# Optimization experiments

Hardware: AMD Instinct MI355X
Metric: run time of the kernel (lower is better)

Reference implementation:

```python
import jax, jax.numpy as jnp
import numpy as np
import math

B, L = 16, 100
NC = 80
STRIDES = (8.0, 16.0, 32.0)
ANCHORS = np.array([[10., 13.], [16., 30.], [33., 23.], [30., 61.], [62., 45.],
                    [59., 119.], [116., 90.], [156., 198.], [373., 326.]], np.float32)
ANCH_MASKS = ((0, 1, 2), (3, 4, 5), (6, 7, 8))
THRESH = 4.0          # gt_match_max_ratio
CIOU_RATIO = 1.0
W_BOX, W_OBJ, W_CLS = 0.05, 1.0, 0.58
OV = 0.5              # overlap in assign_targets_to_proposals


def _bce(x, z):
    # binary_cross_entropy_with_logits, elementwise
    return -(z * jax.nn.log_sigmoid(x) + (1.0 - z) * jax.nn.log_sigmoid(-x))


def _ciou_xywh(b1, b2, eps=1e-9):
    # b1, b2: [M,4] center-x, center-y, w, h  (matches _bbox_iou with x1y1x2y2=False, CIoU=True)
    b1x1, b1x2 = b1[:, 0] - b1[:, 2] / 2, b1[:, 0] + b1[:, 2] / 2
    b1y1, b1y2 = b1[:, 1] - b1[:, 3] / 2, b1[:, 1] + b1[:, 3] / 2
    b2x1, b2x2 = b2[:, 0] - b2[:, 2] / 2, b2[:, 0] + b2[:, 2] / 2
    b2y1, b2y2 = b2[:, 1] - b2[:, 3] / 2, b2[:, 1] + b2[:, 3] / 2
    inter = jnp.clip(jnp.minimum(b1x2, b2x2) - jnp.maximum(b1x1, b2x1), 0) * \
            jnp.clip(jnp.minimum(b1y2, b2y2) - jnp.maximum(b1y1, b2y1), 0)
    w1, h1 = b1x2 - b1x1, b1y2 - b1y1 + eps
    w2, h2 = b2x2 - b2x1, b2y2 - b2y1 + eps
    union = w1 * h1 + w2 * h2 - inter + eps
    iou = inter / union
    cw = jnp.maximum(b1x2, b2x2) - jnp.minimum(b1x1, b2x1)
    ch = jnp.maximum(b1y2, b2y2) - jnp.minimum(b1y1, b2y1)
    c2 = cw ** 2 + ch ** 2 + eps
    rho2 = ((b2x1 + b2x2 - b1x1 - b1x2) ** 2 + (b2y1 + b2y2 - b1y1 - b1y2) ** 2) / 4
    v = (4.0 / math.pi ** 2) * (jnp.arctan(w2 / h2) - jnp.arctan(w1 / h1)) ** 2
    alpha = jax.lax.stop_gradient(v / (1.0 + eps - iou + v))  # torch.no_grad()
    return iou - (rho2 / c2 + v * alpha)


def _yolo_loss(y_pred0, y_pred1, y_pred2, y_true):
    # valid GT rows: nlabel counts rows with positive sum; valid rows assumed contiguous at front
    nlabel = (y_true.sum(-1) > 0).sum(-1)                                # [B]
    valid = (jnp.arange(L)[None, :] < nlabel[:, None]).reshape(-1)       # [N]
    batch_ids = jnp.repeat(jnp.arange(B), L)                             # [N]
    flat = y_true.reshape(-1, 5)
    gt_labels = flat[:, 4].astype(jnp.int32)
    # convert x1,y1,w,h -> cx,cy,w,h
    gt_boxes = jnp.concatenate([flat[:, :2] + flat[:, 2:4] / 2, flat[:, 2:4]], axis=1)
    N = B * L
    offsets = jnp.array([[0, 0], [-OV, 0], [0, -OV], [OV, 0], [0, OV]], jnp.float32)
    loss_box = jnp.float32(0.0)
    loss_obj = jnp.float32(0.0)
    loss_cls = jnp.float32(0.0)
    for li, out in enumerate((y_pred0, y_pred1, y_pred2)):
        s = STRIDES[li]
        anch = jnp.asarray(ANCHORS[list(ANCH_MASKS[li])] / s)            # [3,2] grid units
        H, Wd = out.shape[2], out.shape[3]
        nch = 5 + NC
        p = out.reshape(B, -1, nch, H, Wd).transpose(0, 1, 3, 4, 2)      # [B,3,H,W,nch]
        sgb = gt_boxes / s                                               # [N,4]
        # size_matched_idx
        r = sgb[:, None, 2:4] / anch[None]                               # [N,3,2]
        maxr = jnp.maximum(r, 1.0 / r).max(-1)                           # [N,3]
        match = (maxr < THRESH) & valid[:, None]                         # [N,3]
        # assign_targets_to_proposals: 5 offset candidates per (gt, anchor)
        x, y = sgb[:, 0], sgb[:, 1]
        fx, fy = jnp.mod(x, 1.0), jnp.mod(y, 1.0)
        cond = jnp.stack([
            jnp.ones_like(x, bool),
            (x > 1) & (fx < OV),
            (y > 1) & (fy < OV),
            (x < Wd - 1) & (fx > 1 - OV),
            (y < H - 1) & (fy > 1 - OV),
        ], axis=1)                                                       # [N,5]
        coords = (sgb[:, None, :2] + offsets[None]).astype(jnp.int32)    # [N,5,2] (trunc like .long())
        cmask = (match[:, :, None] & cond[:, None, :]).reshape(-1)       # [N*3*5]
        bf = jnp.broadcast_to(batch_ids[:, None, None], (N, 3, 5)).reshape(-1)
        af = jnp.broadcast_to(jnp.arange(3)[None, :, None], (N, 3, 5)).reshape(-1)
        gf = jnp.broadcast_to(jnp.arange(N)[:, None, None], (N, 3, 5)).reshape(-1)
        gxy = jnp.broadcast_to(coords[:, None, :, :], (N, 3, 5, 2)).reshape(-1, 2)
        gx, gy = gxy[:, 0], gxy[:, 1]
        pred = p[bf, af, gy, gx]                                         # [M,nch] (OOB gathers clamped; masked out)
        pxy = jax.nn.sigmoid(pred[:, :2]) + gxy.astype(pred.dtype)
        pwh = jnp.exp(pred[:, 2:4]) * anch[af]
        pbox = jnp.concatenate([pxy, pwh], axis=1)
        ci = _ciou_xywh(pbox, sgb[gf])                                   # [M]
        cm = cmask.astype(pred.dtype)
        nval = cm.sum()
        denom = jnp.maximum(nval, 1.0)
        loss_box = loss_box + jnp.where(nval > 0, ((1.0 - ci) * cm).sum() / denom, 0.0)
        # objectness target scatter (invalid candidates dropped via OOB batch index)
        obj_val = CIOU_RATIO * jnp.clip(ci, 0) + (1.0 - CIOU_RATIO)
        bs = jnp.where(cmask, bf, B)
        gt_obj = jnp.zeros((B, 3, H, Wd), pred.dtype).at[bs, af, gy, gx].set(obj_val, mode='drop')
        if NC > 1:
            zhot = jax.nn.one_hot(gt_labels[gf], NC, dtype=pred.dtype)
            bce_c = _bce(pred[:, 5:], zhot)
            loss_cls = loss_cls + jnp.where(nval > 0, (bce_c * cm[:, None]).sum() / (denom * NC), 0.0)
        loss_obj = loss_obj + _bce(p[..., 4], gt_obj).mean()
    lb, lo, lc = W_BOX * loss_box, W_OBJ * loss_obj, W_CLS * loss_cls
    return lb + lo + lc, lb, lo, lc


def setup_inputs():
    rng = np.random.default_rng(0)
    k0, k1, k2 = jax.random.split(jax.random.key(0), 3)
    y_pred0 = jax.random.normal(k0, (B, 3 * (5 + NC), 80, 80), jnp.float32)
    y_pred1 = jax.random.normal(k1, (B, 3 * (5 + NC), 40, 40), jnp.float32)
    y_pred2 = jax.random.normal(k2, (B, 3 * (5 + NC), 20, 20), jnp.float32)
    yt = np.zeros((B, L, 5), np.float32)
    n_valid = 70  # valid labels contiguous at the front, rest zero-padded
    yt[:, :n_valid, 0] = rng.uniform(1.0, 560.0, (B, n_valid))
    yt[:, :n_valid, 1] = rng.uniform(1.0, 560.0, (B, n_valid))
    yt[:, :n_valid, 2] = rng.uniform(8.0, 80.0, (B, n_valid))
    yt[:, :n_valid, 3] = rng.uniform(8.0, 80.0, (B, n_valid))
    yt[:, :n_valid, 4] = rng.integers(0, NC, (B, n_valid)).astype(np.float32)
    return {"y_pred0": y_pred0, "y_pred1": y_pred1, "y_pred2": y_pred2, "y_true": jnp.asarray(yt)}


def reference(y_pred0, y_pred1, y_pred2, y_true):
    return _yolo_loss(y_pred0, y_pred1, y_pred2, y_true)
```

## Files before the change

kernel.cpp:

```cpp
#include <hip/hip_runtime.h>
#include <math.h>

#define BB 16
#define LL 100
#define NCLS 80
#define CPB 282
#define CAP 288
#define PREPB 256
#define GATB 4608
#define OBJB 99
#define NTHR 1024

__device__ __constant__ int   d_W[3]     = {80, 40, 20};
__device__ __constant__ int   d_HW[3]    = {6400, 1600, 400};
__device__ __constant__ float d_stride[3]= {8.f, 16.f, 32.f};
__device__ __constant__ int   d_gtoff[3] = {0, 307200, 384000};
__device__ __constant__ float d_anch[3][3][2] = {
  {{10.f,13.f},{16.f,30.f},{33.f,23.f}},
  {{30.f,61.f},{62.f,45.f},{59.f,119.f}},
  {{116.f,90.f},{156.f,198.f},{373.f,326.f}}};

#define ACC_OFF   0
#define CNT_OFF   16
#define CANDG_OFF 272

__device__ __forceinline__ float softplusf(float t) {
  return fmaxf(t, 0.f) + log1pf(expf(-fabsf(t)));
}
__device__ __forceinline__ float sigmoidf_(float x) {
  return 1.f / (1.f + expf(-x));
}

__device__ __forceinline__ float ciou_(float px, float py, float pw, float ph,
                                       float gx, float gy, float gw, float gh) {
  const float eps = 1e-9f;
  float b1x1 = px - pw*0.5f, b1x2 = px + pw*0.5f;
  float b1y1 = py - ph*0.5f, b1y2 = py + ph*0.5f;
  float b2x1 = gx - gw*0.5f, b2x2 = gx + gw*0.5f;
  float b2y1 = gy - gh*0.5f, b2y2 = gy + gh*0.5f;
  float iw = fmaxf(fminf(b1x2,b2x2) - fmaxf(b1x1,b2x1), 0.f);
  float ih = fmaxf(fminf(b1y2,b2y2) - fmaxf(b1y1,b2y1), 0.f);
  float inter = iw*ih;
  float w1 = b1x2-b1x1, h1 = b1y2-b1y1 + eps;
  float w2 = b2x2-b2x1, h2 = b2y2-b2y1 + eps;
  float uni = w1*h1 + w2*h2 - inter + eps;
  float iou = inter/uni;
  float cw = fmaxf(b1x2,b2x2) - fminf(b1x1,b2x1);
  float ch = fmaxf(b1y2,b2y2) - fminf(b1y1,b2y1);
  float c2 = cw*cw + ch*ch + eps;
  float dx = b2x1+b2x2-b1x1-b1x2;
  float dy = b2y1+b2y2-b1y1-b1y2;
  float rho2 = (dx*dx + dy*dy)*0.25f;
  float at = atanf(w2/h2) - atanf(w1/h1);
  float v = (float)(4.0/(M_PI*M_PI)) * at*at;
  float alpha = v / (1.0f + eps - iou + v);
  return iou - (rho2/c2 + v*alpha);
}

__global__ __launch_bounds__(512)
void k_prep(const float* __restrict__ yt, float* __restrict__ acc,
            unsigned int* __restrict__ cntg, unsigned int* __restrict__ candg)
{
  __shared__ int s_nl[2];
  __shared__ int s_cnt;
  const int blk = blockIdx.x, tid = threadIdx.x;

  if (blk == 0 && tid >= 32 && tid < 48) acc[tid-32] = 0.f;

  if (tid < 2)  s_nl[tid] = 0;
  if (tid == 2) s_cnt = 0;

  const int t0 = blk*CPB;
  const int b_lo = t0/4500;
  int b_hi = (t0 + CPB - 1)/4500; if (b_hi > BB-1) b_hi = BB-1;
  __syncthreads();

  if (tid < LL) {
    const float* row = yt + (size_t)(b_lo*LL + tid)*5;
    if (row[0]+row[1]+row[2]+row[3]+row[4] > 0.f) atomicAdd(&s_nl[0], 1);
  } else if (tid >= 128 && tid < 128+LL && b_hi != b_lo) {
    const float* row = yt + (size_t)(b_hi*LL + (tid-128))*5;
    if (row[0]+row[1]+row[2]+row[3]+row[4] > 0.f) atomicAdd(&s_nl[1], 1);
  }
  __syncthreads();

  if (tid < CPB) {
    int t = t0 + tid;
    if (t < BB*LL*45) {
      int b = t/4500; int rem = t - b*4500;
      int g_loc = rem/45; int rem2 = rem - g_loc*45;
      int lvl = rem2/15, ao = rem2 - lvl*15, a = ao/5, o = ao - a*5;
      const float* row = yt + (size_t)(b*LL + g_loc)*5;
      float s = d_stride[lvl];
      int W = d_W[lvl];
      float cx = (row[0] + row[2]*0.5f)/s;
      float cy = (row[1] + row[3]*0.5f)/s;
      float w = row[2]/s, h = row[3]/s;
      float aw = d_anch[lvl][a][0]/s, ah = d_anch[lvl][a][1]/s;
      float rw = w/aw, rh = h/ah;
      float maxr = fmaxf(fmaxf(rw,1.f/rw), fmaxf(rh,1.f/rh));
      int nl = (b == b_lo) ? s_nl[0] : s_nl[1];
      bool m = (g_loc < nl) && (maxr < 4.0f);
      float fx = cx - floorf(cx), fy = cy - floorf(cy);
      bool c;
      switch (o) {
        case 0: c = true; break;
        case 1: c = (cx > 1.f) && (fx < 0.5f); break;
        case 2: c = (cy > 1.f) && (fy < 0.5f); break;
        case 3: c = (cx < (float)(W-1)) && (fx > 0.5f); break;
        default:c = (cy < (float)(W-1)) && (fy > 0.5f); break;
      }
      if (m && c) {
        const float offx[5] = {0.f,-0.5f,0.f,0.5f,0.f};
        const float offy[5] = {0.f,0.f,-0.5f,0.f,0.5f};
        int gx = (int)(cx + offx[o]);
        int gy = (int)(cy + offy[o]);
        int g = b*LL + g_loc;
        unsigned pk = ((unsigned)lvl<<27) | ((unsigned)a<<25) | ((unsigned)g<<14)
                    | ((unsigned)gy<<7) | (unsigned)gx;
        int idx = atomicAdd(&s_cnt, 1);
        candg[blk*CAP + idx] = pk;
      }
    }
  }
  __syncthreads();
  if (tid == 0) cntg[blk] = (unsigned)s_cnt;
}

__global__ __launch_bounds__(NTHR)
void k_gather(const float* __restrict__ p0, const float* __restrict__ p1,
              const float* __restrict__ p2, const float* __restrict__ yt,
              const unsigned int* __restrict__ cntg,
              const unsigned int* __restrict__ candg,
              float* __restrict__ acc)
{
  __shared__ float s_acc[15];
  const int blk = blockIdx.x, tid = threadIdx.x;
  if (tid < 15) s_acc[tid] = 0.f;
  __syncthreads();

  if (blk < GATB) {
    int wg = blk*16 + (tid >> 6);
    int lane = tid & 63;
    int p = wg / CAP;
    int sIdx = wg - p*CAP;
    if (sIdx < (int)cntg[p]) {
      unsigned pk = candg[p*CAP + sIdx];
      int gx  = pk & 127;
      int gy  = (pk>>7) & 127;
      int g   = (pk>>14) & 2047;
      int a   = (pk>>25) & 3;
      int lvl = (pk>>27) & 3;
      int b = g / LL;
      float s = d_stride[lvl];
      int W = d_W[lvl], HW = d_HW[lvl];
      const float* pr = (lvl==0) ? p0 : (lvl==1) ? p1 : p2;
      const float* row = yt + (size_t)g*5;
      float cx = (row[0] + row[2]*0.5f)/s;
      float cy = (row[1] + row[3]*0.5f)/s;
      float w  = row[2]/s, h = row[3]/s;
      int label = (int)row[4];
      float aw = d_anch[lvl][a][0]/s, ah = d_anch[lvl][a][1]/s;

      const float* base = pr + (size_t)((b*255 + a*85)*HW + gy*W + gx);
      float xA = base[(size_t)lane*HW];
      float xB = (lane < 21) ? base[(size_t)(64+lane)*HW] : 0.f;
      float x0 = __shfl(xA,0), x1 = __shfl(xA,1), x2 = __shfl(xA,2), x3 = __shfl(xA,3);
      float xobj = __shfl(xA,4);

      float pxc = sigmoidf_(x0) + (float)gx;
      float pyc = sigmoidf_(x1) + (float)gy;
      float pw = expf(x2)*aw, ph = expf(x3)*ah;
      float ci = ciou_(pxc,pyc,pw,ph, cx,cy,w,h);

      float cls = 0.f;
      if (lane >= 5) { int cc = lane-5;  cls += (cc==label) ? softplusf(-xA) : softplusf(xA); }
      if (lane < 21) { int cc = 59+lane; cls += (cc==label) ? softplusf(-xB) : softplusf(xB); }
      for (int off = 1; off < 64; off <<= 1) cls += __shfl_xor(cls, off);

      if (lane == 0) {
        float bx = 1.f - ci;
        float zx = fmaxf(ci, 0.f) * xobj;
        atomicAdd(&s_acc[lvl],     bx);
        atomicAdd(&s_acc[3+lvl],  cls);
        atomicAdd(&s_acc[6+lvl],  1.f);
        atomicAdd(&s_acc[12+lvl], zx);
      }
    }
  } else {
    int gt = (blk - GATB)*NTHR + tid;
    if (gt < 100800) {
      int e0 = gt*4;
      int lvl = (e0 < 307200) ? 0 : (e0 < 384000 ? 1 : 2);
      int HW = d_HW[lvl];
      int idx = e0 - d_gtoff[lvl];
      int b = idx/(3*HW); int r2 = idx - b*3*HW; int a = r2/HW; int pos = r2 - a*HW;
      const float* pr = (lvl==0) ? p0 : (lvl==1) ? p1 : p2;
      const float4 x4 = *(const float4*)(pr + (size_t)((b*255 + a*85 + 4)*HW + pos));
      float sp = softplusf(x4.x) + softplusf(x4.y) + softplusf(x4.z) + softplusf(x4.w);
      atomicAdd(&s_acc[9+(e0 < 307200 ? 0 : (e0 < 384000 ? 1 : 2))], sp);
    }
  }
  __syncthreads();
  if (tid < 15 && s_acc[tid] != 0.f) atomicAdd(&acc[tid], s_acc[tid]);
}

__global__ __launch_bounds__(64)
void k_fin(const float* __restrict__ acc, float* __restrict__ out) {
  if (threadIdx.x != 0) return;
  const float cells[3] = {307200.f, 76800.f, 19200.f};
  float lb = 0.f, lc = 0.f, lo = 0.f;
  for (int l = 0; l < 3; ++l) {
    float nval  = acc[6+l];
    float denom = fmaxf(nval, 1.f);
    if (nval > 0.f) {
      lb += acc[l] / denom;
      lc += acc[3+l] / (denom * (float)NCLS);
    }
    lo += (acc[9+l] - acc[12+l]) / cells[l];
  }
  lb *= 0.05f;
  lc *= 0.58f;
  out[0] = lb + lo + lc;
  out[1] = lb;
  out[2] = lo;
  out[3] = lc;
}

extern "C" void kernel_launch(void* const* d_in, const int* in_sizes, int n_in,
                              void* d_out, int out_size, void* d_ws, size_t ws_size,
                              hipStream_t stream) {
  const float* p0 = (const float*)d_in[0];
  const float* p1 = (const float*)d_in[1];
  const float* p2 = (const float*)d_in[2];
  const float* yt = (const float*)d_in[3];

  float*        wsf   = (float*)d_ws;
  float*        acc   = wsf + ACC_OFF;
  unsigned int* cntg  = (unsigned int*)(wsf + CNT_OFF);
  unsigned int* candg = (unsigned int*)(wsf + CANDG_OFF);

  k_prep  <<<PREPB, 512, 0, stream>>>(yt, acc, cntg, candg);
  k_gather<<<GATB + OBJB, NTHR, 0, stream>>>(p0, p1, p2, yt, cntg, candg, acc);
  k_fin   <<<1, 64, 0, stream>>>(acc, (float*)d_out);
}
```

Baseline: 47.44 us.

## Compute class BCE via per-cell positive counts and streamed softplus sums

```diff
diff --git a/kernel.cpp b/kernel.cpp
--- a/kernel.cpp
+++ b/kernel.cpp
@@ -7,8 +7,8 @@
 #define CPB 282
 #define CAP 288
 #define PREPB 256
+#define STRB 768
 #define GATB 4608
-#define OBJB 99
 #define NTHR 1024
 
 __device__ __constant__ int   d_W[3]     = {80, 40, 20};
@@ -23,6 +23,7 @@
 #define ACC_OFF   0
 #define CNT_OFF   16
 #define CANDG_OFF 272
+#define COUNT_OFF 74000
 
 __device__ __forceinline__ float softplusf(float t) {
   return fmaxf(t, 0.f) + log1pf(expf(-fabsf(t)));
@@ -57,9 +58,16 @@
   return iou - (rho2/c2 + v*alpha);
 }
 
+__global__ __launch_bounds__(256)
+void k_zero(uint4* __restrict__ cnt4) {
+  int t = blockIdx.x*256 + threadIdx.x;
+  if (t < 100800) cnt4[t] = make_uint4(0u,0u,0u,0u);
+}
+
 __global__ __launch_bounds__(512)
 void k_prep(const float* __restrict__ yt, float* __restrict__ acc,
-            unsigned int* __restrict__ cntg, unsigned int* __restrict__ candg)
+            unsigned int* __restrict__ cntg, unsigned int* __restrict__ candg,
+            unsigned int* __restrict__ count)
 {
   __shared__ int s_nl[2];
   __shared__ int s_cnt;
@@ -120,6 +128,7 @@
                     | ((unsigned)gy<<7) | (unsigned)gx;
         int idx = atomicAdd(&s_cnt, 1);
         candg[blk*CAP + idx] = pk;
+        atomicAdd(&count[d_gtoff[lvl] + (b*3 + a)*d_HW[lvl] + gy*W + gx], 1u);
       }
     }
   }
@@ -128,19 +137,59 @@
 }
 
 __global__ __launch_bounds__(NTHR)
-void k_gather(const float* __restrict__ p0, const float* __restrict__ p1,
-              const float* __restrict__ p2, const float* __restrict__ yt,
-              const unsigned int* __restrict__ cntg,
-              const unsigned int* __restrict__ candg,
-              float* __restrict__ acc)
+void k_main(const float* __restrict__ p0, const float* __restrict__ p1,
+            const float* __restrict__ p2, const float* __restrict__ yt,
+            const unsigned int* __restrict__ cntg,
+            const unsigned int* __restrict__ candg,
+            const unsigned int* __restrict__ count,
+            float* __restrict__ acc)
 {
   __shared__ float s_acc[15];
   const int blk = blockIdx.x, tid = threadIdx.x;
   if (tid < 15) s_acc[tid] = 0.f;
   __syncthreads();
 
-  if (blk < GATB) {
-    int wg = blk*16 + (tid >> 6);
+  if (blk < STRB) {
+    int lvl, tile, chunk, part;
+    if (blk < 384)      { lvl = 0; tile = blk >> 3; int r = blk & 7; chunk = r >> 2; part = r & 3; }
+    else if (blk < 576) { lvl = 1; int r = blk - 384; tile = r >> 2; chunk = 0; part = r & 3; }
+    else                { lvl = 2; int r = blk - 576; tile = r >> 2; chunk = 0; part = r & 3; }
+    int b = tile / 3, a = tile - 3*(tile/3);
+    int HW = d_HW[lvl];
+    int pos0 = chunk*4096 + tid*4;
+    float so = 0.f, clsp = 0.f;
+    if (pos0 < HW) {
+      const float* pr = (lvl==0) ? p0 : (lvl==1) ? p1 : p2;
+      const float* base = pr + (size_t)(b*255 + a*85)*HW + pos0;
+      const uint4 c4 = *(const uint4*)(count + d_gtoff[lvl] + (b*3 + a)*HW + pos0);
+      bool any = (c4.x | c4.y | c4.z | c4.w) != 0u;
+      int cs = (part == 0) ? 4 : (5 + 20*part);
+      int ce = 25 + 20*part;
+      float4 S = make_float4(0.f,0.f,0.f,0.f);
+      for (int c = cs; c < ce; ++c) {
+        const float4 x4 = *(const float4*)(base + (size_t)c*HW);
+        if (c == 4) {
+          so = softplusf(x4.x) + softplusf(x4.y) + softplusf(x4.z) + softplusf(x4.w);
+        } else if (any) {
+          if (c4.x) S.x += softplusf(x4.x);
+          if (c4.y) S.y += softplusf(x4.y);
+          if (c4.z) S.z += softplusf(x4.z);
+          if (c4.w) S.w += softplusf(x4.w);
+        }
+      }
+      if (any)
+        clsp = (float)c4.x*S.x + (float)c4.y*S.y + (float)c4.z*S.z + (float)c4.w*S.w;
+    }
+    for (int off = 1; off < 64; off <<= 1) {
+      so   += __shfl_xor(so, off);
+      clsp += __shfl_xor(clsp, off);
+    }
+    if ((tid & 63) == 0) {
+      if (so   != 0.f) atomicAdd(&s_acc[9+lvl], so);
+      if (clsp != 0.f) atomicAdd(&s_acc[3+lvl], clsp);
+    }
+  } else {
+    int wg = (blk - STRB)*16 + (tid >> 6);
     int lane = tid & 63;
     int p = wg / CAP;
     int sIdx = wg - p*CAP;
@@ -163,42 +212,28 @@
       float aw = d_anch[lvl][a][0]/s, ah = d_anch[lvl][a][1]/s;
 
       const float* base = pr + (size_t)((b*255 + a*85)*HW + gy*W + gx);
-      float xA = base[(size_t)lane*HW];
-      float xB = (lane < 21) ? base[(size_t)(64+lane)*HW] : 0.f;
-      float x0 = __shfl(xA,0), x1 = __shfl(xA,1), x2 = __shfl(xA,2), x3 = __shfl(xA,3);
-      float xobj = __shfl(xA,4);
+      float xv = 0.f;
+      if (lane < 6) {
+        int ch = (lane < 5) ? lane : (5 + label);
+        xv = base[(size_t)ch*HW];
+      }
+      float x0 = __shfl(xv,0), x1 = __shfl(xv,1), x2 = __shfl(xv,2), x3 = __shfl(xv,3);
+      float xobj = __shfl(xv,4);
+      float xl   = __shfl(xv,5);
 
       float pxc = sigmoidf_(x0) + (float)gx;
       float pyc = sigmoidf_(x1) + (float)gy;
       float pw = expf(x2)*aw, ph = expf(x3)*ah;
       float ci = ciou_(pxc,pyc,pw,ph, cx,cy,w,h);
 
-      float cls = 0.f;
-      if (lane >= 5) { int cc = lane-5;  cls += (cc==label) ? softplusf(-xA) : softplusf(xA); }
-      if (lane < 21) { int cc = 59+lane; cls += (cc==label) ? softplusf(-xB) : softplusf(xB); }
-      for (int off = 1; off < 64; off <<= 1) cls += __shfl_xor(cls, off);
-
       if (lane == 0) {
         float bx = 1.f - ci;
         float zx = fmaxf(ci, 0.f) * xobj;
-        atomicAdd(&s_acc[lvl],     bx);
-        atomicAdd(&s_acc[3+lvl],  cls);
-        atomicAdd(&s_acc[6+lvl],  1.f);
-        atomicAdd(&s_acc[12+lvl], zx);
-      }
-    }
-  } else {
-    int gt = (blk - GATB)*NTHR + tid;
-    if (gt < 100800) {
-      int e0 = gt*4;
-      int lvl = (e0 < 307200) ? 0 : (e0 < 384000 ? 1 : 2);
-      int HW = d_HW[lvl];
-      int idx = e0 - d_gtoff[lvl];
-      int b = idx/(3*HW); int r2 = idx - b*3*HW; int a = r2/HW; int pos = r2 - a*HW;
-      const float* pr = (lvl==0) ? p0 : (lvl==1) ? p1 : p2;
-      const float4 x4 = *(const float4*)(pr + (size_t)((b*255 + a*85 + 4)*HW + pos));
-      float sp = softplusf(x4.x) + softplusf(x4.y) + softplusf(x4.z) + softplusf(x4.w);
-      atomicAdd(&s_acc[9+(e0 < 307200 ? 0 : (e0 < 384000 ? 1 : 2))], sp);
+        atomicAdd(&s_acc[lvl],      bx);
+        atomicAdd(&s_acc[3+lvl],  -xl);
+        atomicAdd(&s_acc[6+lvl],   1.f);
+        atomicAdd(&s_acc[12+lvl],  zx);
+      }
     }
   }
   __syncthreads();
@@ -239,8 +274,10 @@
   float*        acc   = wsf + ACC_OFF;
   unsigned int* cntg  = (unsigned int*)(wsf + CNT_OFF);
   unsigned int* candg = (unsigned int*)(wsf + CANDG_OFF);
-
-  k_prep  <<<PREPB, 512, 0, stream>>>(yt, acc, cntg, candg);
-  k_gather<<<GATB + OBJB, NTHR, 0, stream>>>(p0, p1, p2, yt, cntg, candg, acc);
-  k_fin   <<<1, 64, 0, stream>>>(acc, (float*)d_out);
-}
+  unsigned int* count = (unsigned int*)(wsf + COUNT_OFF);
+
+  k_zero<<<394, 256, 0, stream>>>((uint4*)count);
+  k_prep<<<PREPB, 512, 0, stream>>>(yt, acc, cntg, candg, count);
+  k_main<<<STRB + GATB, NTHR, 0, stream>>>(p0, p1, p2, yt, cntg, candg, count, acc);
+  k_fin <<<1, 64, 0, stream>>>(acc, (float*)d_out);
+}
```

Result: slower. 159.6 us (+236.4%).
